# Kernel optimization log

Hardware: AMD Instinct MI355X
Metric: run time of the kernel (lower is better)

Reference implementation:

```python
import jax, jax.numpy as jnp
import numpy as np

DN = ('NHWC', 'HWIO', 'NHWC')

def _conv1x1(x, k):
    # 1x1 conv, stride 1, SAME padding (channels_last)
    return jax.lax.conv_general_dilated(x, k, window_strides=(1, 1), padding='SAME', dimension_numbers=DN)

def setup_inputs() -> dict:
    key = jax.random.key(0)
    k1, k2, k3, k4, k5 = jax.random.split(key, 5)
    B, H, W, C = 4, 64, 64, 256
    c8 = C // 8
    x = jax.random.normal(k1, (B, H, W, C), dtype=jnp.float32)
    # Glorot-like scaling for stability
    kernel_f = jax.random.normal(k2, (1, 1, C, c8), dtype=jnp.float32) * (1.0 / np.sqrt(C))
    kernel_g = jax.random.normal(k3, (1, 1, C, c8), dtype=jnp.float32) * (1.0 / np.sqrt(C))
    kernel_h = jax.random.normal(k4, (1, 1, C, C), dtype=jnp.float32) * (1.0 / np.sqrt(C))
    gamma = jax.random.normal(k5, (), dtype=jnp.float32) * 0.1
    return {'x': x, 'kernel_f': kernel_f, 'kernel_g': kernel_g, 'kernel_h': kernel_h, 'gamma': gamma}

def reference(x, kernel_f, kernel_g, kernel_h, gamma):
    B, H, W, C = x.shape
    N = H * W
    f = _conv1x1(x, kernel_f).reshape(B, N, -1)   # [B, N, C/8] queries
    g = _conv1x1(x, kernel_g).reshape(B, N, -1)   # [B, N, C/8] keys
    h = _conv1x1(x, kernel_h).reshape(B, N, -1)   # [B, N, C]   values
    e = jnp.einsum('bnc,bmc->bnm', f, g)          # [B, N, N] scores
    attn = jax.nn.softmax(e, axis=-1)
    o = jnp.einsum('bnm,bmc->bnc', attn, h).reshape(B, H, W, C)
    return x + gamma * o
```

## Files before the change

kernel.cpp:

```cpp
#include <hip/hip_runtime.h>

typedef __attribute__((ext_vector_type(8))) short bf16x8;
typedef __attribute__((ext_vector_type(4))) float f32x4;
typedef __attribute__((ext_vector_type(16))) float f32x16;

__device__ __forceinline__ unsigned short f2bf(float f) {
    union { float f; unsigned u; } v; v.f = f;
    return (unsigned short)((v.u + 0x7FFFu + ((v.u >> 16) & 1u)) >> 16);
}

__device__ __forceinline__ float fexp2(float v) {
#if __has_builtin(__builtin_amdgcn_exp2f)
    return __builtin_amdgcn_exp2f(v);
#else
    float r; asm("v_exp_f32 %0, %1" : "=v"(r) : "v"(v)); return r;
#endif
}
__device__ __forceinline__ unsigned cvt_pk_bf16(float lo, float hi) {
    unsigned r;
    asm("v_cvt_pk_bf16_f32 %0, %1, %2" : "=v"(r) : "v"(lo), "v"(hi));
    return r;
}

__device__ __forceinline__ void async16(unsigned short* lds, const unsigned short* gsrc) {
    __builtin_amdgcn_global_load_lds(
        (const __attribute__((address_space(1))) void*)gsrc,
        (__attribute__((address_space(3))) void*)lds, 16, 0, 0);
}

__global__ __launch_bounds__(256) void k_wt(const float* __restrict__ kf,
                                            const float* __restrict__ kg,
                                            const float* __restrict__ kh,
                                            unsigned short* __restrict__ wt) {
    int n = blockIdx.x, t = threadIdx.x;
    const float* src; int stride, col;
    if (n < 32)      { src = kf; stride = 32;  col = n; }
    else if (n < 64) { src = kg; stride = 32;  col = n - 32; }
    else             { src = kh; stride = 256; col = n - 64; }
    float v = src[t * stride + col];
    if (n < 32) v *= 1.44269504088896341f;
    wt[n * 256 + (((t >> 3) ^ (n & 7)) << 3) + (t & 7)] = f2bf(v);
}

__global__ __launch_bounds__(512) void k_proj(const float* __restrict__ x,
                                              const unsigned short* __restrict__ wt,
                                              unsigned short* __restrict__ f,
                                              unsigned short* __restrict__ g,
                                              unsigned short* __restrict__ hT) {
    __shared__ unsigned short xs[8192];
    __shared__ unsigned short ws[16384];
    int t = threadIdx.x, rb = blockIdx.x;
    int w = t >> 6, lane = t & 63, q = lane >> 4, n15 = lane & 15;
    int b = rb >> 7, nbase = (rb & 127) * 32;
    int rg0 = w & 1, cg0 = w >> 1;
    int cgh = w & 3, rgh = w >> 2;

#pragma unroll
    for (int i = 0; i < 4; ++i) {
        int lin = i * 512 + t, row = lin >> 6, c4 = lin & 63;
        float4 v = *(const float4*)&x[(rb * 32 + row) * 256 + c4 * 4];
        ushort4 o; o.x = f2bf(v.x); o.y = f2bf(v.y); o.z = f2bf(v.z); o.w = f2bf(v.w);
        *(ushort4*)&xs[row * 256 + (((c4 >> 1) ^ (row & 7)) << 3) + ((c4 & 1) << 2)] = o;
    }
#pragma unroll
    for (int j = 0; j < 4; ++j)
        async16(&ws[(j * 512 + w * 64) * 8], wt + (j * 512 + t) * 8);
    __syncthreads();

    for (int ct = 0; ct < 5; ++ct) {
        f32x4 acc = (f32x4){0.f, 0.f, 0.f, 0.f};
        if (ct == 0) {
#pragma unroll
            for (int kk = 0; kk < 8; ++kk) {
                bf16x8 a = *(const bf16x8*)&xs[(rg0 * 16 + n15) * 256
                                + ((((kk << 2) + q) ^ (n15 & 7)) << 3)];
                bf16x8 bw = *(const bf16x8*)&ws[(cg0 * 16 + n15) * 256
                                + ((((kk << 2) + q) ^ (n15 & 7)) << 3)];
                acc = __builtin_amdgcn_mfma_f32_16x16x32_bf16(a, bw, acc, 0, 0, 0);
            }
        } else {
#pragma unroll
            for (int kk = 0; kk < 8; ++kk) {
                bf16x8 a = *(const bf16x8*)&ws[(cgh * 16 + n15) * 256
                                + ((((kk << 2) + q) ^ (n15 & 7)) << 3)];
                bf16x8 bx = *(const bf16x8*)&xs[(rgh * 16 + n15) * 256
                                + ((((kk << 2) + q) ^ (n15 & 7)) << 3)];
                acc = __builtin_amdgcn_mfma_f32_16x16x32_bf16(a, bx, acc, 0, 0, 0);
            }
        }
        __syncthreads();
        if (ct < 4) {
            const unsigned short* wsrc = wt + (ct + 1) * 16384;
#pragma unroll
            for (int j = 0; j < 4; ++j)
                async16(&ws[(j * 512 + w * 64) * 8], wsrc + (j * 512 + t) * 8);
        }
        if (ct == 0) {
#pragma unroll
            for (int r = 0; r < 4; ++r) {
                int grow = rb * 32 + rg0 * 16 + q * 4 + r;
                int col = cg0 * 16 + n15;
                unsigned short v = f2bf(acc[r]);
                if (col < 32) f[grow * 32 + col] = v;
                else          g[grow * 32 + (col - 32)] = v;
            }
        } else {
#pragma unroll
            for (int r = 0; r < 4; ++r) {
                int ch = (ct - 1) * 64 + cgh * 16 + q * 4 + r;
                hT[b * 1048576 + ch * 4096 + nbase + rgh * 16 + n15] = f2bf(acc[r]);
            }
        }
        __syncthreads();
    }
}

__global__ __launch_bounds__(512, 4) void k_attn(const float* __restrict__ x,
                                                 const unsigned short* __restrict__ f,
                                                 const unsigned short* __restrict__ g,
                                                 const unsigned short* __restrict__ hT,
                                                 const float* __restrict__ gamma_p,
                                                 float* __restrict__ out) {
    __shared__ unsigned short hs[3][8192];
    __shared__ unsigned short pls[2][4096];
    __shared__ float lpart[4][64];
    __shared__ __align__(16) float lrec[64];
    int t = threadIdx.x, bx = blockIdx.x;
    int b = (bx >> 1) & 3;
    int ch2 = (bx >> 3) & 1;
    int qt = ((bx & 1) << 5) | (bx >> 4);
    int qbase = qt * 64;
    int chbase = ch2 * 128;
    int w = t >> 6, l = t & 63;
    int hi = l >> 5, l31 = l & 31;
    int q = l >> 4, n15 = l & 15;
    int cb = w & 3;
    const bool is_s = (w < 4);

    bf16x8 aFB[4];
    const unsigned short* gW = g + (b * 4096 + w * 16 + n15) * 32 + q * 8;
    if (is_s) {
#pragma unroll
        for (int nt = 0; nt < 4; ++nt)
            aFB[nt] = *(const bf16x8*)&f[(b * 4096 + qbase + nt * 16 + n15) * 32 + q * 8];
    }
    bf16x8 aG, aGn;
    f32x4 lac = (f32x4){0.f, 0.f, 0.f, 0.f};
    const f32x4 zero4 = (f32x4){0.f, 0.f, 0.f, 0.f};

    const unsigned short* hsrc = hT + b * 1048576 + (chbase + (t >> 3)) * 4096
                               + (((t & 7) ^ ((t >> 3) & 7)) << 3);

    auto s_tile = [&](int buf) {
        f32x4 sa[4];
#pragma unroll
        for (int nt = 0; nt < 4; ++nt)
            sa[nt] = __builtin_amdgcn_mfma_f32_16x16x32_bf16(aG, aFB[nt], zero4, 0, 0, 0);
        int kq = w * 4 + q;
#pragma unroll
        for (int nt = 0; nt < 4; ++nt) {
#pragma unroll
            for (int r = 0; r < 4; ++r) {
                sa[nt][r] = fexp2(sa[nt][r]);
                lac[nt] += sa[nt][r];
            }
            unsigned p0 = cvt_pk_bf16(sa[nt][0], sa[nt][1]);
            unsigned p1 = cvt_pk_bf16(sa[nt][2], sa[nt][3]);
            int row = nt * 16 + n15;
            unsigned* dst = (unsigned*)&pls[buf][row * 64]
                          + (((kq >> 1) ^ (n15 & 7)) << 2) + ((kq & 1) << 1);
            dst[0] = p0; dst[1] = p1;
        }
    };

    f32x16 o0, o1;
#pragma unroll
    for (int i = 0; i < 16; ++i) { o0[i] = 0.f; o1[i] = 0.f; }

    async16(&hs[0][w * 512], hsrc);
    async16(&hs[0][4096 + w * 512], hsrc + 64 * 4096);
    async16(&hs[1][w * 512], hsrc + 64);
    async16(&hs[1][4096 + w * 512], hsrc + 64 * 4096 + 64);
    if (is_s) {
        aG  = *(const bf16x8*)&gW[0];
        aGn = *(const bf16x8*)&gW[2048];
        s_tile(0);
        aG = aGn;
        __builtin_amdgcn_sched_barrier(0);
        asm volatile("s_waitcnt vmcnt(3) lgkmcnt(0)" ::: "memory");
    } else {
        __builtin_amdgcn_sched_barrier(0);
        asm volatile("s_waitcnt vmcnt(2)" ::: "memory");
    }
    __builtin_amdgcn_s_barrier();
    __builtin_amdgcn_sched_barrier(0);

    for (int kt = 0; kt < 64; ++kt) {
        int cur = kt & 1, nxt = cur ^ 1;
        int h_cur = kt % 3, h_nxt2 = (kt + 2) % 3;
        const bool more = (kt + 2 < 64);

        if (more) {
            const unsigned short* hp = hsrc + (kt + 2) * 64;
            async16(&hs[h_nxt2][w * 512], hp);
            async16(&hs[h_nxt2][4096 + w * 512], hp + 64 * 4096);
        }

        if (is_s) {
            if (kt + 1 < 64) {
                int ktn = (kt + 2 < 64) ? kt + 2 : 63;
                aGn = *(const bf16x8*)&gW[ktn * 2048];
                s_tile(nxt);
                aG = aGn;
            }
            __builtin_amdgcn_sched_barrier(0);
            if (more) asm volatile("s_waitcnt vmcnt(3) lgkmcnt(0)" ::: "memory");
            else      asm volatile("s_waitcnt vmcnt(1) lgkmcnt(0)" ::: "memory");
        } else {
            const unsigned short* hcur = &hs[h_cur][0];
            const unsigned short* pcur = &pls[cur][0];
            __builtin_amdgcn_s_setprio(1);
#pragma unroll
            for (int ks = 0; ks < 4; ++ks) {
                int seg = (((2 * ks + hi) ^ (l31 & 7)) << 3);
                bf16x8 bH  = *(const bf16x8*)&hcur[(cb * 32 + l31) * 64 + seg];
                bf16x8 aP0 = *(const bf16x8*)&pcur[l31 * 64 + seg];
                bf16x8 aP1 = *(const bf16x8*)&pcur[(32 + l31) * 64 + seg];
                o0 = __builtin_amdgcn_mfma_f32_32x32x16_bf16(aP0, bH, o0, 0, 0, 0);
                o1 = __builtin_amdgcn_mfma_f32_32x32x16_bf16(aP1, bH, o1, 0, 0, 0);
            }
            __builtin_amdgcn_s_setprio(0);
            __builtin_amdgcn_sched_barrier(0);
            if (more) asm volatile("s_waitcnt vmcnt(2)" ::: "memory");
            else      asm volatile("s_waitcnt vmcnt(0)" ::: "memory");
        }

        __builtin_amdgcn_s_barrier();
        __builtin_amdgcn_sched_barrier(0);
    }

    if (is_s) {
#pragma unroll
        for (int nt = 0; nt < 4; ++nt) {
            float ps = lac[nt];
            ps += __shfl_xor(ps, 16);
            ps += __shfl_xor(ps, 32);
            if (q == 0) lpart[w][nt * 16 + n15] = ps;
        }
    }
    __syncthreads();
    if (t < 64) lrec[t] = 1.0f / (lpart[0][t] + lpart[1][t] + lpart[2][t] + lpart[3][t]);
    __syncthreads();
    if (!is_s) {
        float gam = *gamma_p;
        int ch = chbase + cb * 32 + l31;
#pragma unroll
        for (int qq = 0; qq < 4; ++qq) {
            int r0 = 8 * qq + 4 * hi;
            f32x4 ri0 = *(const f32x4*)&lrec[r0];
            f32x4 ri1 = *(const f32x4*)&lrec[32 + r0];
#pragma unroll
            for (int j = 0; j < 4; ++j) {
                int idx0 = (b * 4096 + qbase + r0 + j) * 256 + ch;
                int idx1 = idx0 + 32 * 256;
                out[idx0] = x[idx0] + gam * (o0[4 * qq + j] * ri0[j]);
                out[idx1] = x[idx1] + gam * (o1[4 * qq + j] * ri1[j]);
            }
        }
    }
}

extern "C" void kernel_launch(void* const* d_in, const int* in_sizes, int n_in,
                              void* d_out, int out_size, void* d_ws, size_t ws_size,
                              hipStream_t stream) {
    const float* x  = (const float*)d_in[0];
    const float* kf = (const float*)d_in[1];
    const float* kg = (const float*)d_in[2];
    const float* kh = (const float*)d_in[3];
    const float* gm = (const float*)d_in[4];
    float* out = (float*)d_out;

    char* ws = (char*)d_ws;
    unsigned short* wt = (unsigned short*)(ws);
    unsigned short* fb = (unsigned short*)(ws + 163840);
    unsigned short* gb = (unsigned short*)(ws + 1212416);
    unsigned short* hT = (unsigned short*)(ws + 2260992);

    hipLaunchKernelGGL(k_wt,   dim3(320), dim3(256), 0, stream, kf, kg, kh, wt);
    hipLaunchKernelGGL(k_proj, dim3(512), dim3(512), 0, stream, x, wt, fb, gb, hT);
    hipLaunchKernelGGL(k_attn, dim3(512), dim3(512), 0, stream, x, fb, gb, hT, gm, out);
}
```

Before: 151.2 us.

## Load value tiles directly into registers with key-blocked hT layout, drop LDS staging

The projection kernel now writes the value matrix in a key-blocked layout (8 keys × 256 channels per block), so each PV wave can fetch its MFMA B-operand fragments straight from global memory into registers. This removes the triple-buffered LDS staging of h, its async copies and the vmcnt waits, and prefetches the next tile into registers one iteration ahead. In exchange there is more register pressure and a direct dependence on global/L2 latency being hidden within one iteration. LDS use also drops, which may allow more occupancy.

After: 136.6 us (median of 2 runs). 9.7% less time.

```diff
diff --git a/kernel.cpp b/kernel.cpp
--- a/kernel.cpp
+++ b/kernel.cpp
@@ -108,7 +108,8 @@
 #pragma unroll
             for (int r = 0; r < 4; ++r) {
                 int ch = (ct - 1) * 64 + cgh * 16 + q * 4 + r;
-                hT[b * 1048576 + ch * 4096 + nbase + rgh * 16 + n15] = f2bf(acc[r]);
+                int key = nbase + rgh * 16 + n15;
+                hT[((b * 512 + (key >> 3)) * 256 + ch) * 8 + (key & 7)] = f2bf(acc[r]);
             }
         }
         __syncthreads();
@@ -121,7 +122,6 @@
                                                  const unsigned short* __restrict__ hT,
                                                  const float* __restrict__ gamma_p,
                                                  float* __restrict__ out) {
-    __shared__ unsigned short hs[3][8192];
     __shared__ unsigned short pls[2][4096];
     __shared__ float lpart[4][64];
     __shared__ __align__(16) float lrec[64];
@@ -148,8 +148,9 @@
     f32x4 lac = (f32x4){0.f, 0.f, 0.f, 0.f};
     const f32x4 zero4 = (f32x4){0.f, 0.f, 0.f, 0.f};
 
-    const unsigned short* hsrc = hT + b * 1048576 + (chbase + (t >> 3)) * 4096
-                               + (((t & 7) ^ ((t >> 3) & 7)) << 3);
+    const unsigned short* hb2 = hT + b * 1048576
+                              + (chbase + cb * 32 + l31) * 8 + hi * 2048;
+    bf16x8 bHc[4], bHn[4];
 
     auto s_tile = [&](int buf) {
         f32x4 sa[4];
@@ -177,34 +178,25 @@
 #pragma unroll
     for (int i = 0; i < 16; ++i) { o0[i] = 0.f; o1[i] = 0.f; }
 
-    async16(&hs[0][w * 512], hsrc);
-    async16(&hs[0][4096 + w * 512], hsrc + 64 * 4096);
-    async16(&hs[1][w * 512], hsrc + 64);
-    async16(&hs[1][4096 + w * 512], hsrc + 64 * 4096 + 64);
     if (is_s) {
         aG  = *(const bf16x8*)&gW[0];
         aGn = *(const bf16x8*)&gW[2048];
         s_tile(0);
         aG = aGn;
         __builtin_amdgcn_sched_barrier(0);
-        asm volatile("s_waitcnt vmcnt(3) lgkmcnt(0)" ::: "memory");
+        asm volatile("s_waitcnt lgkmcnt(0)" ::: "memory");
     } else {
+#pragma unroll
+        for (int ks = 0; ks < 4; ++ks)
+            bHc[ks] = *(const bf16x8*)&hb2[ks * 4096];
         __builtin_amdgcn_sched_barrier(0);
-        asm volatile("s_waitcnt vmcnt(2)" ::: "memory");
     }
     __builtin_amdgcn_s_barrier();
     __builtin_amdgcn_sched_barrier(0);
 
+#pragma unroll 2
     for (int kt = 0; kt < 64; ++kt) {
         int cur = kt & 1, nxt = cur ^ 1;
-        int h_cur = kt % 3, h_nxt2 = (kt + 2) % 3;
-        const bool more = (kt + 2 < 64);
-
-        if (more) {
-            const unsigned short* hp = hsrc + (kt + 2) * 64;
-            async16(&hs[h_nxt2][w * 512], hp);
-            async16(&hs[h_nxt2][4096 + w * 512], hp + 64 * 4096);
-        }
 
         if (is_s) {
             if (kt + 1 < 64) {
@@ -214,25 +206,29 @@
                 aG = aGn;
             }
             __builtin_amdgcn_sched_barrier(0);
-            if (more) asm volatile("s_waitcnt vmcnt(3) lgkmcnt(0)" ::: "memory");
-            else      asm volatile("s_waitcnt vmcnt(1) lgkmcnt(0)" ::: "memory");
+            asm volatile("s_waitcnt lgkmcnt(0)" ::: "memory");
         } else {
-            const unsigned short* hcur = &hs[h_cur][0];
+            if (kt + 1 < 64) {
+#pragma unroll
+                for (int ks = 0; ks < 4; ++ks)
+                    bHn[ks] = *(const bf16x8*)&hb2[(kt + 1) * 16384 + ks * 4096];
+            }
             const unsigned short* pcur = &pls[cur][0];
             __builtin_amdgcn_s_setprio(1);
 #pragma unroll
             for (int ks = 0; ks < 4; ++ks) {
                 int seg = (((2 * ks + hi) ^ (l31 & 7)) << 3);
-                bf16x8 bH  = *(const bf16x8*)&hcur[(cb * 32 + l31) * 64 + seg];
                 bf16x8 aP0 = *(const bf16x8*)&pcur[l31 * 64 + seg];
                 bf16x8 aP1 = *(const bf16x8*)&pcur[(32 + l31) * 64 + seg];
-                o0 = __builtin_amdgcn_mfma_f32_32x32x16_bf16(aP0, bH, o0, 0, 0, 0);
-                o1 = __builtin_amdgcn_mfma_f32_32x32x16_bf16(aP1, bH, o1, 0, 0, 0);
+                o0 = __builtin_amdgcn_mfma_f32_32x32x16_bf16(aP0, bHc[ks], o0, 0, 0, 0);
+                o1 = __builtin_amdgcn_mfma_f32_32x32x16_bf16(aP1, bHc[ks], o1, 0, 0, 0);
             }
             __builtin_amdgcn_s_setprio(0);
+            if (kt + 1 < 64) {
+#pragma unroll
+                for (int ks = 0; ks < 4; ++ks) bHc[ks] = bHn[ks];
+            }
             __builtin_amdgcn_sched_barrier(0);
-            if (more) asm volatile("s_waitcnt vmcnt(2)" ::: "memory");
-            else      asm volatile("s_waitcnt vmcnt(0)" ::: "memory");
         }
 
         __builtin_amdgcn_s_barrier();
```
